# Optimization experiments

Hardware: AMD Instinct MI355X
Metric: run time of the kernel (lower is better)

Reference implementation:

```python
import jax, jax.numpy as jnp
import numpy as np

EPS = 1e-8
CMAP_SHARPNESS = 100.0  # sigmoid sharpness in contact_map_of_m_to_n


def setup_inputs() -> dict:
    key = jax.random.key(0)
    k1, k2, k3, k4 = jax.random.split(key, 4)
    N, M, V, F = 8192, 4096, 2048, 2048
    obj_points = jax.random.normal(k1, (N, 3), jnp.float32)
    sr_points = 0.8 * jax.random.normal(k2, (M, 3), jnp.float32)
    verts = 0.8 * jax.random.normal(k3, (V, 3), jnp.float32)
    faces = jax.random.randint(k4, (F, 3), 0, V)
    tri = verts[faces]                                   # [F,3,3]
    fn = jnp.cross(tri[:, 1] - tri[:, 0], tri[:, 2] - tri[:, 0])
    face_normals = fn / (jnp.linalg.norm(fn, axis=-1, keepdims=True) + EPS)
    return {"obj_points": obj_points, "sr_points": sr_points,
            "verts": verts, "faces": faces, "face_normals": face_normals}


def _ray_triangle_hits(origins, dirs, tri, face_normals):
    """Plane-intersection + barycentric inside test. Returns [F,N] bool hits (t>=0)."""
    v0 = tri[:, 0]                                       # [F,3]
    denom = jnp.einsum('fc,nc->fn', face_normals, dirs)  # [F,N]
    safe = jnp.where(jnp.abs(denom) < EPS, EPS, denom)
    num = (jnp.einsum('fc,fc->f', face_normals, v0)[:, None]
           - jnp.einsum('fc,nc->fn', face_normals, origins))
    t = num / safe                                       # [F,N]
    p = origins[None, :, :] + t[..., None] * dirs[None, :, :]  # [F,N,3]
    inside = jnp.ones(t.shape, dtype=bool)
    for i in range(3):  # fixed 3 triangle edges
        vi = tri[:, i]
        vj = tri[:, (i + 1) % 3]
        c = jnp.cross((vj - vi)[:, None, :], p - vi[:, None, :])  # [F,N,3]
        inside = inside & (jnp.einsum('fnc,fc->fn', c, face_normals) >= 0.0)
    return inside & (t >= 0.0) & (jnp.abs(denom) >= EPS)


def reference(obj_points, sr_points, verts, faces, face_normals):
    # get_NN: brute-force nearest sampled hand point for each object point
    d2 = jnp.sum((obj_points[:, None, :] - sr_points[None, :, :]) ** 2, axis=-1)  # [N,M]
    nn_idx = jnp.argmin(d2, axis=1)                      # [N]
    trg_pts = sr_points[nn_idx]                          # batched_index_select
    ray_dirs = trg_pts - obj_points                      # [N,3]
    tri = verts[faces]                                   # v[f] -> [F,3,3]
    hits = _ray_triangle_hits(obj_points, ray_dirs, tri, face_normals)  # [F,N]
    hit_number = jnp.sum(hits.astype(jnp.int32), axis=0)
    interior_mask = (hit_number % 2) != 0                # [N]
    # torch.norm(trg_pts[mask] - obj_points[mask]) == Frobenius norm over masked rows
    pen_dist = jnp.sqrt(jnp.sum(jnp.where(interior_mask[:, None], ray_dirs, 0.0) ** 2))
    # contact_map_of_m_to_n: per-obj-point contact value from NN distance
    nn_dist = jnp.sqrt(jnp.min(d2, axis=1) + EPS)
    cmap = 1.0 - 2.0 * (jax.nn.sigmoid(CMAP_SHARPNESS * nn_dist) - 0.5)
    return pen_dist, cmap
```

## Files before the change

### kernel.cpp

```cpp
#include <hip/hip_runtime.h>
#include <hip/hip_bf16.h>
#include <math.h>

#define EPSF 1e-8f

constexpr int N_OBJ  = 8192;
constexpr int M_SR   = 4096;
constexpr int N_FACE = 2048;

constexpr size_t OFF_FD  = 2ull * N_OBJ * sizeof(float4);
constexpr size_t OFF_PEN = OFF_FD + (size_t)N_FACE * 16 * sizeof(float);
constexpr size_t OFF_BM  = OFF_PEN + (size_t)N_OBJ * sizeof(float);

constexpr int SRTILE  = 2048;
constexpr int NN_PPW  = 4;
constexpr int NN_PPB  = NN_PPW * 4;
constexpr int NN_NBLK = N_OBJ / NN_PPB;
constexpr int SETUP_BLKS = N_FACE / 256;

__global__ __launch_bounds__(256, 4) void d1_nn_setup(
    const float* __restrict__ obj, const float* __restrict__ srp,
    const float* __restrict__ verts, const int* __restrict__ faces,
    const float* __restrict__ fnorm, float* __restrict__ fd,
    float* __restrict__ out, float4* __restrict__ ptrec,
    float* __restrict__ pend2)
{
    const int b   = blockIdx.x;
    const int tid = threadIdx.x;

    if (b >= NN_NBLK) {
        int f = (b - NN_NBLK) * 256 + tid;
        int i0 = faces[3 * f + 0], i1 = faces[3 * f + 1], i2 = faces[3 * f + 2];
        float ax = verts[3 * i0 + 0], ay = verts[3 * i0 + 1], az = verts[3 * i0 + 2];
        float bx = verts[3 * i1 + 0], by = verts[3 * i1 + 1], bz = verts[3 * i1 + 2];
        float cx = verts[3 * i2 + 0], cy = verts[3 * i2 + 1], cz = verts[3 * i2 + 2];
        float fx = fnorm[3 * f + 0], fy = fnorm[3 * f + 1], fz = fnorm[3 * f + 2];
        float nf = fx * ax + fy * ay + fz * az;

        float e0x = bx - ax, e0y = by - ay, e0z = bz - az;
        float g0x = fy * e0z - fz * e0y, g0y = fz * e0x - fx * e0z, g0z = fx * e0y - fy * e0x;
        float h0  = g0x * ax + g0y * ay + g0z * az;
        float e1x = cx - bx, e1y = cy - by, e1z = cz - bz;
        float g1x = fy * e1z - fz * e1y, g1y = fz * e1x - fx * e1z, g1z = fx * e1y - fy * e1x;
        float h1  = g1x * bx + g1y * by + g1z * bz;
        float e2x = ax - cx, e2y = ay - cy, e2z = az - cz;
        float g2x = fy * e2z - fz * e2y, g2y = fz * e2x - fx * e2z, g2z = fx * e2y - fy * e2x;
        float h2  = g2x * cx + g2y * cy + g2z * cz;

        float* o = fd + f * 16;
        o[0] = fx;  o[1] = fy;  o[2] = fz;  o[3] = nf;
        o[4] = g0x; o[5] = g0y; o[6] = g0z; o[7] = h0;
        o[8] = g1x; o[9] = g1y; o[10] = g1z; o[11] = h1;
        o[12] = g2x; o[13] = g2y; o[14] = g2z; o[15] = h2;
        return;
    }

    __shared__ float4 s4[SRTILE];
    const int w    = tid >> 6;
    const int lane = tid & 63;
    const int pbase = b * NN_PPB + w * NN_PPW;

    float ox[NN_PPW], oy[NN_PPW], oz[NN_PPW], oo[NN_PPW], best[NN_PPW];
    int bi[NN_PPW];
#pragma unroll
    for (int q = 0; q < NN_PPW; ++q) {
        int n = pbase + q;
        ox[q] = obj[3 * n]; oy[q] = obj[3 * n + 1]; oz[q] = obj[3 * n + 2];
        oo[q] = ox[q] * ox[q] + oy[q] * oy[q] + oz[q] * oz[q];
        best[q] = 3.4e38f; bi[q] = 0;
    }

    for (int t0 = 0; t0 < M_SR; t0 += SRTILE) {
        __syncthreads();
        for (int i = tid; i < SRTILE; i += 256) {
            float sx = srp[3 * (t0 + i) + 0];
            float sy = srp[3 * (t0 + i) + 1];
            float sz = srp[3 * (t0 + i) + 2];
            s4[i] = make_float4(sx, sy, sz, sx * sx + sy * sy + sz * sz);
        }
        __syncthreads();
#pragma unroll 2
        for (int j = 0; j < SRTILE / 64; ++j) {
            int s = j * 64 + lane;
            float4 v = s4[s];
#pragma unroll
            for (int q = 0; q < NN_PPW; ++q) {
                float m = v.w - 2.0f * (ox[q] * v.x + oy[q] * v.y + oz[q] * v.z);
                if (m < best[q]) { best[q] = m; bi[q] = t0 + s; }
            }
        }
    }
    for (int off = 1; off < 64; off <<= 1) {
#pragma unroll
        for (int q = 0; q < NN_PPW; ++q) {
            float od = __shfl_xor(best[q], off);
            int   oi = __shfl_xor(bi[q], off);
            if (od < best[q] || (od == best[q] && oi < bi[q])) { best[q] = od; bi[q] = oi; }
        }
    }
    if (lane == 0) {
#pragma unroll
        for (int q = 0; q < NN_PPW; ++q) {
            int n = pbase + q;
            float d2 = best[q] + oo[q];
            float dx = srp[3 * bi[q]] - ox[q];
            float dy = srp[3 * bi[q] + 1] - oy[q];
            float dz = srp[3 * bi[q] + 2] - oz[q];
            ptrec[2 * n]     = make_float4(ox[q], oy[q], oz[q], d2);
            ptrec[2 * n + 1] = make_float4(dx, dy, dz, 0.0f);
            pend2[n] = d2;
            out[1 + n] = 2.0f / (1.0f + expf(100.0f * sqrtf(d2 + EPSF)));
        }
    }
}

constexpr int FK_SPLITS = 64;
constexpr int FK_PTBLK  = N_OBJ / 256;
constexpr int FK_NBLK   = FK_PTBLK * FK_SPLITS;

__global__ __launch_bounds__(256, 8) void d2_face(
    const float* __restrict__ fd, const float4* __restrict__ ptrec,
    unsigned long long* __restrict__ bm)
{
    const int tid   = threadIdx.x;
    const int w     = tid >> 6;
    const int lane  = tid & 63;
    const int fs    = blockIdx.x & (FK_SPLITS - 1);
    const int ptblk = blockIdx.x >> 6;
    const int p     = ptblk * 256 + tid;

    float4 r0 = ptrec[2 * p];
    float4 r1 = ptrec[2 * p + 1];
    const float ox = r0.x, oy = r0.y, oz = r0.z;
    const float dx = r1.x, dy = r1.y, dz = r1.z;

    const float4* __restrict__ c4 = (const float4*)fd + (size_t)(fs * 32) * 4;

    int cnt = 0;
#pragma unroll 4
    for (int j = 0; j < 32; ++j) {
        float4 q0 = c4[4 * j + 0];
        float den = q0.x * dx + q0.y * dy + q0.z * dz;
        float num = q0.w - (q0.x * ox + q0.y * oy + q0.z * oz);
        float Px  = den * ox + num * dx;
        float Py  = den * oy + num * dy;
        float Pz  = den * oz + num * dz;
        bool pos = den >= 0.0f;

        float4 q1 = c4[4 * j + 1];
        bool ok0 = ((q1.x * Px + q1.y * Py + q1.z * Pz - den * q1.w) >= 0.0f) == pos;
        float4 q2 = c4[4 * j + 2];
        bool ok1 = ((q2.x * Px + q2.y * Py + q2.z * Pz - den * q2.w) >= 0.0f) == pos;
        float4 q3 = c4[4 * j + 3];
        bool ok2 = ((q3.x * Px + q3.y * Py + q3.z * Pz - den * q3.w) >= 0.0f) == pos;

        bool tok = (num >= 0.0f) == pos;
        bool aok = fabsf(den) >= EPSF;
        cnt += (ok0 & ok1 & ok2 & tok & aok) ? 1 : 0;
    }

    unsigned long long m = __ballot((cnt & 1) != 0);
    if (lane == 0) bm[(size_t)fs * 128 + ptblk * 4 + w] = m;
}

__global__ __launch_bounds__(256) void d3_fin(
    const float* __restrict__ pend2, const unsigned long long* __restrict__ bm,
    float* __restrict__ out)
{
    __shared__ float wsum[4];
    const int t = threadIdx.x;
    float s = 0.0f;
    if (t < 128) {
        unsigned long long x = 0;
#pragma unroll
        for (int fs = 0; fs < FK_SPLITS; ++fs) x ^= bm[(size_t)fs * 128 + t];
        const float4* p4 = (const float4*)(pend2 + t * 64);
#pragma unroll
        for (int k = 0; k < 16; ++k) {
            float4 v = p4[k];
            unsigned int nib = (unsigned int)(x >> (4 * k)) & 0xFu;
            s += (nib & 1u) ? v.x : 0.0f;
            s += (nib & 2u) ? v.y : 0.0f;
            s += (nib & 4u) ? v.z : 0.0f;
            s += (nib & 8u) ? v.w : 0.0f;
        }
    }
    for (int off = 1; off < 64; off <<= 1) s += __shfl_xor(s, off);
    if ((t & 63) == 0) wsum[t >> 6] = s;
    __syncthreads();
    if (t == 0) out[0] = sqrtf(wsum[0] + wsum[1] + wsum[2] + wsum[3]);
}

extern "C" void kernel_launch(void* const* d_in, const int* in_sizes, int n_in,
                              void* d_out, int out_size, void* d_ws, size_t ws_size,
                              hipStream_t stream)
{
    const float* obj   = (const float*)d_in[0];
    const float* srp   = (const float*)d_in[1];
    const float* verts = (const float*)d_in[2];
    const int*   faces = (const int*)d_in[3];
    const float* fnorm = (const float*)d_in[4];
    float*       out   = (float*)d_out;

    float4*             ptrec = (float4*)d_ws;
    float*              fd    = (float*)((char*)d_ws + OFF_FD);
    float*              pend2 = (float*)((char*)d_ws + OFF_PEN);
    unsigned long long* bm    = (unsigned long long*)((char*)d_ws + OFF_BM);

    d1_nn_setup<<<NN_NBLK + SETUP_BLKS, 256, 0, stream>>>(obj, srp, verts, faces, fnorm,
                                                          fd, out, ptrec, pend2);
    d2_face<<<FK_NBLK, 256, 0, stream>>>(fd, ptrec, bm);
    d3_fin<<<1, 256, 0, stream>>>(pend2, bm, out);
}
```

Measured before the change: 38.29 us.

## Split NN search over two halves of hand points and merge in face kernel

```diff
diff --git a/kernel.cpp b/kernel.cpp
--- a/kernel.cpp
+++ b/kernel.cpp
@@ -8,22 +8,22 @@
 constexpr int M_SR   = 4096;
 constexpr int N_FACE = 2048;
 
-constexpr size_t OFF_FD  = 2ull * N_OBJ * sizeof(float4);
-constexpr size_t OFF_PEN = OFF_FD + (size_t)N_FACE * 16 * sizeof(float);
-constexpr size_t OFF_BM  = OFF_PEN + (size_t)N_OBJ * sizeof(float);
-
-constexpr int SRTILE  = 2048;
+constexpr size_t OFF_CAND = (size_t)N_FACE * 16 * sizeof(float);
+constexpr size_t OFF_PEN  = OFF_CAND + 2ull * N_OBJ * sizeof(float4);
+constexpr size_t OFF_BM   = OFF_PEN + (size_t)N_OBJ * sizeof(float);
+
+constexpr int SR_HALF = M_SR / 2;
+constexpr int SRTILE  = 1024;
 constexpr int NN_PPW  = 4;
 constexpr int NN_PPB  = NN_PPW * 4;
-constexpr int NN_NBLK = N_OBJ / NN_PPB;
+constexpr int NN_NBLK = (N_OBJ / NN_PPB) * 2;
 constexpr int SETUP_BLKS = N_FACE / 256;
 
-__global__ __launch_bounds__(256, 4) void d1_nn_setup(
+__global__ __launch_bounds__(256) void d1_nn_setup(
     const float* __restrict__ obj, const float* __restrict__ srp,
     const float* __restrict__ verts, const int* __restrict__ faces,
     const float* __restrict__ fnorm, float* __restrict__ fd,
-    float* __restrict__ out, float4* __restrict__ ptrec,
-    float* __restrict__ pend2)
+    float4* __restrict__ cand)
 {
     const int b   = blockIdx.x;
     const int tid = threadIdx.x;
@@ -56,30 +56,32 @@
     }
 
     __shared__ float4 s4[SRTILE];
+    const int half = b & 1;
+    const int ptg  = b >> 1;
     const int w    = tid >> 6;
     const int lane = tid & 63;
-    const int pbase = b * NN_PPB + w * NN_PPW;
-
-    float ox[NN_PPW], oy[NN_PPW], oz[NN_PPW], oo[NN_PPW], best[NN_PPW];
+    const int pbase = ptg * NN_PPB + w * NN_PPW;
+    const float* __restrict__ sbase = srp + 3 * half * SR_HALF;
+
+    float ox[NN_PPW], oy[NN_PPW], oz[NN_PPW], best[NN_PPW];
     int bi[NN_PPW];
 #pragma unroll
     for (int q = 0; q < NN_PPW; ++q) {
         int n = pbase + q;
         ox[q] = obj[3 * n]; oy[q] = obj[3 * n + 1]; oz[q] = obj[3 * n + 2];
-        oo[q] = ox[q] * ox[q] + oy[q] * oy[q] + oz[q] * oz[q];
         best[q] = 3.4e38f; bi[q] = 0;
     }
 
-    for (int t0 = 0; t0 < M_SR; t0 += SRTILE) {
+    for (int t0 = 0; t0 < SR_HALF; t0 += SRTILE) {
         __syncthreads();
         for (int i = tid; i < SRTILE; i += 256) {
-            float sx = srp[3 * (t0 + i) + 0];
-            float sy = srp[3 * (t0 + i) + 1];
-            float sz = srp[3 * (t0 + i) + 2];
+            float sx = sbase[3 * (t0 + i) + 0];
+            float sy = sbase[3 * (t0 + i) + 1];
+            float sz = sbase[3 * (t0 + i) + 2];
             s4[i] = make_float4(sx, sy, sz, sx * sx + sy * sy + sz * sz);
         }
         __syncthreads();
-#pragma unroll 2
+#pragma unroll 4
         for (int j = 0; j < SRTILE / 64; ++j) {
             int s = j * 64 + lane;
             float4 v = s4[s];
@@ -101,15 +103,12 @@
     if (lane == 0) {
 #pragma unroll
         for (int q = 0; q < NN_PPW; ++q) {
-            int n = pbase + q;
-            float d2 = best[q] + oo[q];
-            float dx = srp[3 * bi[q]] - ox[q];
-            float dy = srp[3 * bi[q] + 1] - oy[q];
-            float dz = srp[3 * bi[q] + 2] - oz[q];
-            ptrec[2 * n]     = make_float4(ox[q], oy[q], oz[q], d2);
-            ptrec[2 * n + 1] = make_float4(dx, dy, dz, 0.0f);
-            pend2[n] = d2;
-            out[1 + n] = 2.0f / (1.0f + expf(100.0f * sqrtf(d2 + EPSF)));
+            int n  = pbase + q;
+            int gi = half * SR_HALF + bi[q];
+            float dx = srp[3 * gi + 0] - ox[q];
+            float dy = srp[3 * gi + 1] - oy[q];
+            float dz = srp[3 * gi + 2] - oz[q];
+            cand[half * N_OBJ + n] = make_float4(dx, dy, dz, best[q]);
         }
     }
 }
@@ -118,9 +117,10 @@
 constexpr int FK_PTBLK  = N_OBJ / 256;
 constexpr int FK_NBLK   = FK_PTBLK * FK_SPLITS;
 
-__global__ __launch_bounds__(256, 8) void d2_face(
-    const float* __restrict__ fd, const float4* __restrict__ ptrec,
-    unsigned long long* __restrict__ bm)
+__global__ __launch_bounds__(256, 4) void d2_face(
+    const float* __restrict__ obj, const float* __restrict__ fd,
+    const float4* __restrict__ cand, float* __restrict__ out,
+    float* __restrict__ pend2, unsigned long long* __restrict__ bm)
 {
     const int tid   = threadIdx.x;
     const int w     = tid >> 6;
@@ -129,10 +129,21 @@
     const int ptblk = blockIdx.x >> 6;
     const int p     = ptblk * 256 + tid;
 
-    float4 r0 = ptrec[2 * p];
-    float4 r1 = ptrec[2 * p + 1];
-    const float ox = r0.x, oy = r0.y, oz = r0.z;
-    const float dx = r1.x, dy = r1.y, dz = r1.z;
+    float4 c0 = cand[p];
+    float4 c1 = cand[N_OBJ + p];
+    const bool tb = c1.w < c0.w;
+    const float dx = tb ? c1.x : c0.x;
+    const float dy = tb ? c1.y : c0.y;
+    const float dz = tb ? c1.z : c0.z;
+    const float m  = tb ? c1.w : c0.w;
+
+    const float ox = obj[3 * p], oy = obj[3 * p + 1], oz = obj[3 * p + 2];
+
+    if (fs == 0) {
+        float d2 = m + (ox * ox + oy * oy + oz * oz);
+        pend2[p] = d2;
+        out[1 + p] = 2.0f / (1.0f + expf(100.0f * sqrtf(d2 + EPSF)));
+    }
 
     const float4* __restrict__ c4 = (const float4*)fd + (size_t)(fs * 32) * 4;
 
@@ -159,8 +170,8 @@
         cnt += (ok0 & ok1 & ok2 & tok & aok) ? 1 : 0;
     }
 
-    unsigned long long m = __ballot((cnt & 1) != 0);
-    if (lane == 0) bm[(size_t)fs * 128 + ptblk * 4 + w] = m;
+    unsigned long long msk = __ballot((cnt & 1) != 0);
+    if (lane == 0) bm[(size_t)(ptblk * 4 + w) * 64 + fs] = msk;
 }
 
 __global__ __launch_bounds__(256) void d3_fin(
@@ -168,23 +179,30 @@
     float* __restrict__ out)
 {
     __shared__ float wsum[4];
-    const int t = threadIdx.x;
+    const int t    = threadIdx.x;
+    const int col  = t >> 1;
+    const int half = t & 1;
+
+    const ulonglong2* __restrict__ q2 =
+        (const ulonglong2*)(bm + (size_t)col * 64) + half * 16;
+    unsigned long long x = 0;
+#pragma unroll
+    for (int k = 0; k < 16; ++k) { ulonglong2 v = q2[k]; x ^= v.x ^ v.y; }
+    x ^= __shfl_xor(x, 1);
+
+    unsigned int bits = (unsigned int)(x >> (half * 32));
+    const float4* __restrict__ p4 = (const float4*)(pend2 + (size_t)col * 64 + half * 32);
     float s = 0.0f;
-    if (t < 128) {
-        unsigned long long x = 0;
-#pragma unroll
-        for (int fs = 0; fs < FK_SPLITS; ++fs) x ^= bm[(size_t)fs * 128 + t];
-        const float4* p4 = (const float4*)(pend2 + t * 64);
-#pragma unroll
-        for (int k = 0; k < 16; ++k) {
-            float4 v = p4[k];
-            unsigned int nib = (unsigned int)(x >> (4 * k)) & 0xFu;
-            s += (nib & 1u) ? v.x : 0.0f;
-            s += (nib & 2u) ? v.y : 0.0f;
-            s += (nib & 4u) ? v.z : 0.0f;
-            s += (nib & 8u) ? v.w : 0.0f;
-        }
-    }
+#pragma unroll
+    for (int k = 0; k < 8; ++k) {
+        float4 v = p4[k];
+        unsigned int nib = (bits >> (4 * k)) & 0xFu;
+        s += (nib & 1u) ? v.x : 0.0f;
+        s += (nib & 2u) ? v.y : 0.0f;
+        s += (nib & 4u) ? v.z : 0.0f;
+        s += (nib & 8u) ? v.w : 0.0f;
+    }
+
     for (int off = 1; off < 64; off <<= 1) s += __shfl_xor(s, off);
     if ((t & 63) == 0) wsum[t >> 6] = s;
     __syncthreads();
@@ -202,13 +220,12 @@
     const float* fnorm = (const float*)d_in[4];
     float*       out   = (float*)d_out;
 
-    float4*             ptrec = (float4*)d_ws;
-    float*              fd    = (float*)((char*)d_ws + OFF_FD);
+    float*              fd    = (float*)d_ws;
+    float4*             cand  = (float4*)((char*)d_ws + OFF_CAND);
     float*              pend2 = (float*)((char*)d_ws + OFF_PEN);
     unsigned long long* bm    = (unsigned long long*)((char*)d_ws + OFF_BM);
 
-    d1_nn_setup<<<NN_NBLK + SETUP_BLKS, 256, 0, stream>>>(obj, srp, verts, faces, fnorm,
-                                                          fd, out, ptrec, pend2);
-    d2_face<<<FK_NBLK, 256, 0, stream>>>(fd, ptrec, bm);
+    d1_nn_setup<<<NN_NBLK + SETUP_BLKS, 256, 0, stream>>>(obj, srp, verts, faces, fnorm, fd, cand);
+    d2_face<<<FK_NBLK, 256, 0, stream>>>(obj, fd, cand, out, pend2, bm);
     d3_fin<<<1, 256, 0, stream>>>(pend2, bm, out);
 }
```

Result: faster. 37.13 us (-3.0%).
